# Kernel tuning notes

Hardware: AMD Instinct MI355X
Metric: run time of the kernel (lower is better)

Reference implementation:

```python
import jax, jax.numpy as jnp
import numpy as np

N, E = 50000, 800000          # n_nodes, n_edges
IN_C, OUT_C = 128, 64         # in_channels, out_channels


def setup_inputs() -> dict:
    key = jax.random.key(0)
    ks = jax.random.split(key, 12)
    def w(k, i, o):
        return jax.random.normal(k, (i, o), jnp.float32) / np.float32(np.sqrt(i))
    return {
        "x": jax.random.normal(ks[0], (N, IN_C), jnp.float32),
        "edge_index": jax.random.randint(ks[1], (2, E), 0, N),
        "eps": jax.random.normal(ks[2], (N, OUT_C), jnp.float32),
        # encoder GCNConv1: in -> 2*out
        "W_e1": w(ks[3], IN_C, 2 * OUT_C), "b_e1": jnp.zeros((2 * OUT_C,), jnp.float32),
        # encoder GCNConv2: 2*out -> out
        "W_e2": w(ks[4], 2 * OUT_C, OUT_C), "b_e2": jnp.zeros((OUT_C,), jnp.float32),
        # fc_mu / fc_logvar: out -> out
        "W_mu": w(ks[5], OUT_C, OUT_C), "b_mu": jnp.zeros((OUT_C,), jnp.float32),
        "W_lv": w(ks[6], OUT_C, OUT_C), "b_lv": jnp.zeros((OUT_C,), jnp.float32),
        # decoder GCNConv1: out -> in
        "W_d1": w(ks[7], OUT_C, IN_C), "b_d1": jnp.zeros((IN_C,), jnp.float32),
        # decoder GCNConv2: in -> in
        "W_d2": w(ks[8], IN_C, IN_C), "b_d2": jnp.zeros((IN_C,), jnp.float32),
    }


def _gcn_norm(edge_index, n):
    # PyG gcn_norm: add self-loops, symmetric D^-1/2 A D^-1/2 normalization
    loop = jnp.arange(n)
    src = jnp.concatenate([edge_index[0], loop])
    dst = jnp.concatenate([edge_index[1], loop])
    deg = jax.ops.segment_sum(jnp.ones_like(dst, jnp.float32), dst, num_segments=n)
    dinv = jnp.where(deg > 0, deg ** -0.5, 0.0)
    norm = dinv[src] * dinv[dst]  # [E + N]
    return src, dst, norm


def _gcn_conv(x, W, b, src, dst, norm, n):
    h = x @ W                       # linear transform first (small channel dim)
    msg = h[src] * norm[:, None]    # gather + edge scaling
    return jax.ops.segment_sum(msg, dst, num_segments=n) + b  # scatter-add + bias


def reference(x, edge_index, eps, W_e1, b_e1, W_e2, b_e2, W_mu, b_mu, W_lv, b_lv, W_d1, b_d1, W_d2, b_d2):
    n = x.shape[0]
    src, dst, norm = _gcn_norm(edge_index, n)
    # encoder
    h = jax.nn.relu(_gcn_conv(x, W_e1, b_e1, src, dst, norm, n))
    h = _gcn_conv(h, W_e2, b_e2, src, dst, norm, n)
    mu = h @ W_mu + b_mu
    logvar = h @ W_lv + b_lv
    # reparameterize (training mode)
    z = mu + eps * jnp.exp(0.5 * logvar)
    # decoder
    d = jax.nn.relu(_gcn_conv(z, W_d1, b_d1, src, dst, norm, n))
    d = _gcn_conv(d, W_d2, b_d2, src, dst, norm, n)
    return (d, mu, logvar)
```

## Files before the change

kernel.cpp:

```cpp
#include <hip/hip_runtime.h>
#include <math.h>

typedef unsigned short u16;
typedef unsigned int u32;
typedef __attribute__((ext_vector_type(8))) short s16x8;
typedef __attribute__((ext_vector_type(4))) float f32x4;

__device__ __forceinline__ float bf2f(u16 u) { return __uint_as_float(((u32)u) << 16); }
__device__ __forceinline__ u16 f2bf(float f) {
    u32 u = __float_as_uint(f);
    return (u16)((u + 0x7fffu + ((u >> 16) & 1u)) >> 16);
}

union U4 { u32 u[4]; s16x8 v; };

__device__ __forceinline__ s16x8 pack_hi(f32x4 x0, f32x4 x1) {
    U4 r;
    r.u[0] = (__float_as_uint(x0.y) & 0xFFFF0000u) | (__float_as_uint(x0.x) >> 16);
    r.u[1] = (__float_as_uint(x0.w) & 0xFFFF0000u) | (__float_as_uint(x0.z) >> 16);
    r.u[2] = (__float_as_uint(x1.y) & 0xFFFF0000u) | (__float_as_uint(x1.x) >> 16);
    r.u[3] = (__float_as_uint(x1.w) & 0xFFFF0000u) | (__float_as_uint(x1.z) >> 16);
    return r.v;
}
__device__ __forceinline__ s16x8 pack_lo(f32x4 x0, f32x4 x1) {
    float e0 = x0.x - __uint_as_float(__float_as_uint(x0.x) & 0xFFFF0000u);
    float e1 = x0.y - __uint_as_float(__float_as_uint(x0.y) & 0xFFFF0000u);
    float e2 = x0.z - __uint_as_float(__float_as_uint(x0.z) & 0xFFFF0000u);
    float e3 = x0.w - __uint_as_float(__float_as_uint(x0.w) & 0xFFFF0000u);
    float e4 = x1.x - __uint_as_float(__float_as_uint(x1.x) & 0xFFFF0000u);
    float e5 = x1.y - __uint_as_float(__float_as_uint(x1.y) & 0xFFFF0000u);
    float e6 = x1.z - __uint_as_float(__float_as_uint(x1.z) & 0xFFFF0000u);
    float e7 = x1.w - __uint_as_float(__float_as_uint(x1.w) & 0xFFFF0000u);
    U4 r;
    r.u[0] = (__float_as_uint(e1) & 0xFFFF0000u) | (__float_as_uint(e0) >> 16);
    r.u[1] = (__float_as_uint(e3) & 0xFFFF0000u) | (__float_as_uint(e2) >> 16);
    r.u[2] = (__float_as_uint(e5) & 0xFFFF0000u) | (__float_as_uint(e4) >> 16);
    r.u[3] = (__float_as_uint(e7) & 0xFFFF0000u) | (__float_as_uint(e6) >> 16);
    return r.v;
}

#define BSHIFT 9
#define BSIZE 512
#define BCAP 10240

struct PackArgs { const float* w[6]; };


__device__ __forceinline__ void pack_body(const PackArgs& pa, u16* __restrict__ out, int g, int t) {
    const int Ks[6] = {128, 128, 64, 64, 64, 128};
    const int Ms[6] = {128, 64, 64, 64, 128, 128};
    const int Off[6] = {0, 16384, 24576, 28672, 32768, 40960};
    int s = g >> 6;
    int id = (g & 63) * 256 + t;
    int K = Ks[s], M = Ms[s];
    if (id >= K * M) return;
    int ms = (M == 128) ? 7 : 6;
    int k = id >> ms, c = id & (M - 1);
    int chunk = k >> 5, j = k & 7, lq = (k >> 3) & 3;
    int ct = c >> 4, ln = (c & 15) + (lq << 4);
    out[Off[s] + (chunk * (M >> 4) + ct) * 512 + ln * 8 + j] = f2bf(pa.w[s][id]);
}


__global__ __launch_bounds__(256) void k_bin_pack(const int* __restrict__ ei, int E, int NB, int C,
                                                  int* __restrict__ bin_cursor, u32* __restrict__ binned,
                                                  PackArgs pa, u16* __restrict__ wpk) {
    __shared__ int sh[256];
    const int t = threadIdx.x;
    if ((int)blockIdx.x >= C) {
        pack_body(pa, wpk, blockIdx.x - C, t);
        return;
    }
    int* hist = sh;
    int* base_l = sh + 128;
    const int e0 = blockIdx.x * 4096;
    int sreg[16], dreg[16];
#pragma unroll
    for (int j = 0; j < 16; ++j) {
        int e = e0 + j * 256 + t;
        if (e < E) {
            sreg[j] = ei[e];
            dreg[j] = ei[E + e];
        } else {
            dreg[j] = -1;
        }
    }
    if (t < NB) hist[t] = 0;
    __syncthreads();
#pragma unroll
    for (int j = 0; j < 16; ++j)
        if (dreg[j] >= 0) atomicAdd(&hist[dreg[j] >> BSHIFT], 1);
    __syncthreads();
    if (t < NB) {
        base_l[t] = atomicAdd(&bin_cursor[t], hist[t]);
        hist[t] = 0;
    }
    __syncthreads();
#pragma unroll
    for (int j = 0; j < 16; ++j)
        if (dreg[j] >= 0) {
            int b = dreg[j] >> BSHIFT;
            int pos = base_l[b] + atomicAdd(&hist[b], 1);
            if (pos < BCAP) binned[(size_t)b * BCAP + pos] = ((u32)(dreg[j] & (BSIZE - 1)) << 17) | (u32)sreg[j];
        }
}


template <int K, int M, int RT, int NSET, bool XBF16, bool OUT_BF16, bool BREL>
__device__ __forceinline__ void gemm_tile(const void* __restrict__ Xv, const u16* __restrict__ Bpk,
                                          const float* __restrict__ b0, const float* __restrict__ b1,
                                          const float* __restrict__ eps,
                                          void* __restrict__ Y0, float* __restrict__ Y1,
                                          u16* __restrict__ Z, int N, int col0, int row0, int t) {
    constexpr int CH = K / 32;
    constexpr int TPM = M >> 4;
    constexpr int SETSTRIDE = CH * TPM * 512;
    const int lane = t & 63, w = t >> 6;
    const int l15 = lane & 15, q = lane >> 4;

    s16x8 Bfr[NSET * CH * 4];
#pragma unroll
    for (int s = 0; s < NSET; ++s)
#pragma unroll
        for (int ch = 0; ch < CH; ++ch)
#pragma unroll
            for (int ct = 0; ct < 4; ++ct)
                Bfr[(s * CH + ch) * 4 + ct] =
                    *(const s16x8*)&Bpk[(size_t)s * SETSTRIDE + ((ch * TPM) + (col0 >> 4) + ct) * 512 + lane * 8];

    f32x4 acc[NSET][RT][4];
#pragma unroll
    for (int s = 0; s < NSET; ++s)
#pragma unroll
        for (int rt = 0; rt < RT; ++rt)
#pragma unroll
            for (int ct = 0; ct < 4; ++ct) acc[s][rt][ct] = 0.f;

#pragma unroll
    for (int ch = 0; ch < CH; ++ch) {
#pragma unroll
        for (int rt = 0; rt < RT; ++rt) {
            int r = row0 + (w * RT + rt) * 16 + l15;
            r = r < N ? r : N - 1;
            s16x8 ah, al;
            if (XBF16) {
                ah = *(const s16x8*)((const u16*)Xv + (size_t)r * K + (ch << 5) + (q << 3));
            } else {
                const float* xp = (const float*)Xv + (size_t)r * K + (ch << 5) + (q << 3);
                f32x4 x0 = *(const f32x4*)xp;
                f32x4 x1 = *(const f32x4*)(xp + 4);
                ah = pack_hi(x0, x1);
                al = pack_lo(x0, x1);
            }
#pragma unroll
            for (int s = 0; s < NSET; ++s)
#pragma unroll
                for (int ct = 0; ct < 4; ++ct) {
                    int fb = (s * CH + ch) * 4 + ct;
                    acc[s][rt][ct] = __builtin_amdgcn_mfma_f32_16x16x32_bf16(ah, Bfr[fb], acc[s][rt][ct], 0, 0, 0);
                    if (!XBF16)
                        acc[s][rt][ct] = __builtin_amdgcn_mfma_f32_16x16x32_bf16(al, Bfr[fb], acc[s][rt][ct], 0, 0, 0);
                }
        }
    }

#pragma unroll
    for (int rt = 0; rt < RT; ++rt)
#pragma unroll
        for (int ct = 0; ct < 4; ++ct)
#pragma unroll
            for (int reg = 0; reg < 4; ++reg) {
                int row = row0 + (w * RT + rt) * 16 + q * 4 + reg;
                if (row >= N) continue;
                int col = col0 + ct * 16 + l15;
                if (NSET == 1) {
                    float v = acc[0][rt][ct][reg];
                    if (BREL) v = fmaxf(v + b0[col], 0.f);
                    if (OUT_BF16)
                        ((u16*)Y0)[(size_t)row * M + col] = f2bf(v);
                    else
                        ((float*)Y0)[(size_t)row * M + col] = v;
                } else {
                    float mu = acc[0][rt][ct][reg] + b0[col];
                    float lv = acc[1][rt][ct][reg] + b1[col];
                    size_t o = (size_t)row * 64 + col;
                    ((float*)Y0)[o] = mu;
                    Y1[o] = lv;
                    Z[o] = f2bf(mu + eps[o] * expf(0.5f * lv));
                }
            }
}

template <int K, int M, int RT, int NSET, bool XBF16, bool OUT_BF16, bool BREL>
__global__ __launch_bounds__(256, 3) void k_gemm(const void* __restrict__ Xv, const u16* __restrict__ Bpk,
                                                 const float* __restrict__ b0, const float* __restrict__ b1,
                                                 const float* __restrict__ eps,
                                                 void* __restrict__ Y0, float* __restrict__ Y1,
                                                 u16* __restrict__ Z, int N) {
    gemm_tile<K, M, RT, NSET, XBF16, OUT_BF16, BREL>(Xv, Bpk, b0, b1, eps, Y0, Y1, Z, N,
                                                     blockIdx.x * 64, blockIdx.y * (RT * 64), threadIdx.x);
}


__global__ __launch_bounds__(256, 3) void k_cnt_gemm1(const u32* __restrict__ binned,
                                                      const int* __restrict__ bin_cursor, int N, int NB,
                                                      int* __restrict__ cnt, float* __restrict__ dinv,
                                                      int* __restrict__ row_start, int* __restrict__ cursor,
                                                      const float* __restrict__ x, const u16* __restrict__ wpk,
                                                      u16* __restrict__ R1) {
    __shared__ int cnt_l[BSIZE];
    __shared__ int wave_sum[5];
    __shared__ int base_s;
    const int t = threadIdx.x;
    const int b = blockIdx.x;
    if (b >= NB) {
        gemm_tile<128, 128, 2, 1, false, true, false>(x, wpk, nullptr, nullptr, nullptr, R1, nullptr, nullptr,
                                                      N, 0, (b - NB) * 128, t);
        return;
    }
    const int lane = t & 63, w = t >> 6;
    cnt_l[t] = 0;
    cnt_l[t + 256] = 0;
    __syncthreads();
    const int n = min(bin_cursor[b], BCAP);
    for (int i = t; i < n; i += 256) atomicAdd(&cnt_l[binned[(size_t)b * BCAP + i] >> 17], 1);
    __syncthreads();
    int c0 = cnt_l[2 * t], c1 = cnt_l[2 * t + 1];
    int p0 = (c0 + 7) & ~7, p1 = (c1 + 7) & ~7;
    int s = p0 + p1;
    int incl = s;
#pragma unroll
    for (int o = 1; o < 64; o <<= 1) {
        int v = __shfl_up(incl, o, 64);
        if (lane >= o) incl += v;
    }
    if (lane == 63) wave_sum[w] = incl;
    __syncthreads();
    if (t == 0) {
        int acc = 0;
#pragma unroll
        for (int i = 0; i < 4; ++i) {
            int v = wave_sum[i];
            wave_sum[i] = acc;
            acc += v;
        }
        base_s = atomicAdd(cursor, acc);
    }
    __syncthreads();
    int excl = incl - s + wave_sum[w] + base_s;
    int v0 = b * BSIZE + 2 * t;
    if (v0 < N) {
        cnt[v0] = c0;
        dinv[v0] = rsqrtf((float)(c0 + 1));
        row_start[v0] = excl;
    }
    if (v0 + 1 < N) {
        cnt[v0 + 1] = c1;
        dinv[v0 + 1] = rsqrtf((float)(c1 + 1));
        row_start[v0 + 1] = excl + p0;
    }
}


__global__ __launch_bounds__(256, 3) void k_scat_gemm1(const u32* __restrict__ binned,
                                                       const int* __restrict__ bin_cursor,
                                                       const int* __restrict__ row_start,
                                                       const float* __restrict__ dinv, int N, int NB,
                                                       int2* __restrict__ edges,
                                                       const float* __restrict__ x, const u16* __restrict__ wpk,
                                                       u16* __restrict__ R1) {
    __shared__ float dv_l[BSIZE];
    __shared__ int rs_l[BSIZE];
    __shared__ int fill_l[BSIZE];
    const int t = threadIdx.x;
    const int b = blockIdx.x;
    if (b >= NB) {
        gemm_tile<128, 128, 2, 1, false, true, false>(x, wpk, nullptr, nullptr, nullptr, R1, nullptr, nullptr,
                                                      N, 64, (b - NB) * 128, t);
        return;
    }
#pragma unroll
    for (int hh = 0; hh < 2; ++hh) {
        int d = t + hh * 256;
        int v = b * BSIZE + d;
        bool ok = v < N;
        dv_l[d] = ok ? dinv[v] : 0.f;
        rs_l[d] = ok ? row_start[v] : 0;
        fill_l[d] = 0;
    }
    __syncthreads();
    const int n = min(bin_cursor[b], BCAP);
    for (int i = t; i < n; i += 256) {
        u32 e = binned[(size_t)b * BCAP + i];
        int dl = e >> 17;
        int src = e & 0x1FFFF;
        float wgt = dinv[src] * dv_l[dl];
        int pos = rs_l[dl] + atomicAdd(&fill_l[dl], 1);
        edges[pos] = make_int2(src, __float_as_int(wgt));
    }
    __syncthreads();
#pragma unroll
    for (int hh = 0; hh < 2; ++hh) {
        int d = t + hh * 256;
        int v = b * BSIZE + d;
        if (v >= N) continue;
        int c = fill_l[d];
        int pc = (c + 7) & ~7;
        for (int j = c; j < pc; ++j) edges[rs_l[d] + j] = make_int2(0, 0);
    }
}


template <bool RELU, bool OUT_BF16>
__global__ __launch_bounds__(256) void k_agg128(const u16* __restrict__ hin, const int2* __restrict__ edges,
                                                const int* __restrict__ row_start, const int* __restrict__ cnt,
                                                const float* __restrict__ dinv, const float* __restrict__ bias,
                                                void* __restrict__ out, int N) {
    const int v = blockIdx.x * 4 + (threadIdx.x >> 6);
    const int lane = threadIdx.x & 63;
    if (v >= N) return;
    const int start = __builtin_amdgcn_readfirstlane(row_start[v]);
    const int c = __builtin_amdgcn_readfirstlane(cnt[v]);
    const int pc = (c + 7) & ~7;
    const u32* hp = (const u32*)hin;
    float a0 = 0.f, a1 = 0.f;
    if (pc) {
        int2 e[8];
#pragma unroll
        for (int j = 0; j < 8; ++j) e[j] = edges[start + j];
        for (int i = 0; i < pc; i += 8) {
            u32 h[8];
            float wv[8];
#pragma unroll
            for (int j = 0; j < 8; ++j) {
                h[j] = hp[(size_t)e[j].x * 64 + lane];
                wv[j] = __int_as_float(e[j].y);
            }
            if (i + 8 < pc) {
#pragma unroll
                for (int j = 0; j < 8; ++j) e[j] = edges[start + i + 8 + j];
            }
#pragma unroll
            for (int j = 0; j < 8; ++j) {
                a0 = fmaf(wv[j], bf2f((u16)h[j]), a0);
                a1 = fmaf(wv[j], bf2f((u16)(h[j] >> 16)), a1);
            }
        }
    }
    float dv = dinv[v], sw = dv * dv;
    u32 hs = hp[(size_t)v * 64 + lane];
    a0 = fmaf(sw, bf2f((u16)hs), a0);
    a1 = fmaf(sw, bf2f((u16)(hs >> 16)), a1);
    float2 bp = ((const float2*)bias)[lane];
    a0 += bp.x;
    a1 += bp.y;
    if (RELU) { a0 = fmaxf(a0, 0.f); a1 = fmaxf(a1, 0.f); }
    if (OUT_BF16)
        ((u32*)out)[(size_t)v * 64 + lane] = (u32)f2bf(a0) | ((u32)f2bf(a1) << 16);
    else
        ((float2*)out)[(size_t)v * 64 + lane] = make_float2(a0, a1);
}

template <bool HASB>
__global__ __launch_bounds__(256) void k_agg64(const u16* __restrict__ hin, const int2* __restrict__ edges,
                                               const int* __restrict__ row_start, const int* __restrict__ cnt,
                                               const float* __restrict__ dinv, const float* __restrict__ bias,
                                               float* __restrict__ out, int N) {
    const int v = blockIdx.x * 4 + (threadIdx.x >> 6);
    const int lane = threadIdx.x & 63;
    if (v >= N) return;
    const int start = __builtin_amdgcn_readfirstlane(row_start[v]);
    const int c = __builtin_amdgcn_readfirstlane(cnt[v]);
    const int pc = (c + 7) & ~7;
    float a0 = 0.f;
    if (pc) {
        int2 e[8];
#pragma unroll
        for (int j = 0; j < 8; ++j) e[j] = edges[start + j];
        for (int i = 0; i < pc; i += 8) {
            u16 h[8];
            float wv[8];
#pragma unroll
            for (int j = 0; j < 8; ++j) {
                h[j] = hin[(size_t)e[j].x * 64 + lane];
                wv[j] = __int_as_float(e[j].y);
            }
            if (i + 8 < pc) {
#pragma unroll
                for (int j = 0; j < 8; ++j) e[j] = edges[start + i + 8 + j];
            }
#pragma unroll
            for (int j = 0; j < 8; ++j) a0 = fmaf(wv[j], bf2f(h[j]), a0);
        }
    }
    float dv = dinv[v];
    a0 = fmaf(dv * dv, bf2f(hin[(size_t)v * 64 + lane]), a0);
    if (HASB) a0 += bias[lane];
    out[(size_t)v * 64 + lane] = a0;
}


extern "C" void kernel_launch(void* const* d_in, const int* in_sizes, int n_in,
                              void* d_out, int out_size, void* d_ws, size_t ws_size,
                              hipStream_t stream) {
    const float* x = (const float*)d_in[0];
    const int* ei = (const int*)d_in[1];
    const float* eps = (const float*)d_in[2];
    const float* We1 = (const float*)d_in[3];
    const float* be1 = (const float*)d_in[4];
    const float* We2 = (const float*)d_in[5];
    const float* be2 = (const float*)d_in[6];
    const float* Wmu = (const float*)d_in[7];
    const float* bmu = (const float*)d_in[8];
    const float* Wlv = (const float*)d_in[9];
    const float* blv = (const float*)d_in[10];
    const float* Wd1 = (const float*)d_in[11];
    const float* bd1 = (const float*)d_in[12];
    const float* Wd2 = (const float*)d_in[13];
    const float* bd2 = (const float*)d_in[14];

    const int N = in_sizes[0] / 128;
    const int E = in_sizes[1] / 2;
    const int ECAP = E + 8 * N;
    const int NB = (N + BSIZE - 1) >> BSHIFT;
    const int C = (E + 4095) / 4096;

    int* bin_cursor = (int*)d_ws;
    int* cursor = bin_cursor + 128;
    float* dinv = (float*)(bin_cursor + 256);
    int* row_start = (int*)(dinv + N);
    int* cnt = row_start + N;
    int2* edges = (int2*)(cnt + N);
    u16* R1 = (u16*)(edges + ECAP);
    u16* AZu = R1 + (size_t)N * 128;
    u16* B2 = AZu + (size_t)N * 128;
    u16* Wpk = B2 + (size_t)N * 128;
    float* AZf = (float*)AZu;
    u32* binned = (u32*)AZu;

    float* out_d = (float*)d_out;
    float* out_mu = out_d + (size_t)N * 128;
    float* out_lv = out_mu + (size_t)N * 64;
    float* H2 = out_d;

    hipMemsetAsync(d_ws, 0, 256 * 4, stream);

    PackArgs pa;
    pa.w[0] = We1; pa.w[1] = We2; pa.w[2] = Wmu; pa.w[3] = Wlv; pa.w[4] = Wd1; pa.w[5] = Wd2;

    const int RB128 = (N + 127) / 128;
    const int RB64 = (N + 63) / 64;
    const int AB = (N + 3) / 4;

    k_bin_pack<<<dim3(C + 384), dim3(256), 0, stream>>>(ei, E, NB, C, bin_cursor, binned, pa, Wpk);
    k_cnt_gemm1<<<dim3(NB + RB128), dim3(256), 0, stream>>>(binned, bin_cursor, N, NB, cnt, dinv, row_start,
                                                            cursor, x, Wpk, R1);
    k_scat_gemm1<<<dim3(NB + RB128), dim3(256), 0, stream>>>(binned, bin_cursor, row_start, dinv, N, NB,
                                                             edges, x, Wpk, R1);
    k_agg128<true, true><<<dim3(AB), dim3(256), 0, stream>>>(R1, edges, row_start, cnt, dinv, be1, AZu, N);
    k_gemm<128, 64, 1, 1, true, true, false><<<dim3(1, RB64), dim3(256), 0, stream>>>(AZu, Wpk + 16384, nullptr, nullptr, nullptr, R1, nullptr, nullptr, N);
    k_agg64<true><<<dim3(AB), dim3(256), 0, stream>>>(R1, edges, row_start, cnt, dinv, be2, H2, N);
    k_gemm<64, 64, 1, 2, false, false, false><<<dim3(1, RB64), dim3(256), 0, stream>>>(H2, Wpk + 24576, bmu, blv, eps, out_mu, out_lv, R1, N);
    k_agg64<false><<<dim3(AB), dim3(256), 0, stream>>>(R1, edges, row_start, cnt, dinv, nullptr, AZf, N);
    k_gemm<64, 128, 2, 1, false, true, true><<<dim3(2, RB128), dim3(256), 0, stream>>>(AZf, Wpk + 32768, bd1, nullptr, nullptr, B2, nullptr, nullptr, N);
    k_gemm<128, 128, 2, 1, true, true, false><<<dim3(2, RB128), dim3(256), 0, stream>>>(B2, Wpk + 40960, nullptr, nullptr, nullptr, R1, nullptr, nullptr, N);
    k_agg128<false, false><<<dim3(AB), dim3(256), 0, stream>>>(R1, edges, row_start, cnt, dinv, bd2, out_d, N);
}
```

Baseline: 327.7 us.

## Replace per-node wave aggregation with channel-sliced multi-node aggregation kernel

Merges the two GCN aggregation kernels into one templated kernel. Each wavefront now handles four nodes at once, 16 lanes per node, and the feature channels are split across blocks in 64-byte slices. The intent is to put more independent row gathers in flight per wave and to let the 64-channel layers use packed 32-bit loads instead of 16-bit loads. It drops the software prefetch of edge records and the scalar (readfirstlane) edge indexing, so edge loads become per-lane and nodes in one wave can diverge on degree.

```diff
diff --git a/kernel.cpp b/kernel.cpp
--- a/kernel.cpp
+++ b/kernel.cpp
@@ -311,92 +311,58 @@
 }
 
 
-template <bool RELU, bool OUT_BF16>
-__global__ __launch_bounds__(256) void k_agg128(const u16* __restrict__ hin, const int2* __restrict__ edges,
-                                                const int* __restrict__ row_start, const int* __restrict__ cnt,
-                                                const float* __restrict__ dinv, const float* __restrict__ bias,
-                                                void* __restrict__ out, int N) {
-    const int v = blockIdx.x * 4 + (threadIdx.x >> 6);
-    const int lane = threadIdx.x & 63;
-    if (v >= N) return;
-    const int start = __builtin_amdgcn_readfirstlane(row_start[v]);
-    const int c = __builtin_amdgcn_readfirstlane(cnt[v]);
-    const int pc = (c + 7) & ~7;
+template <int CHU, int SL, bool RELU, bool OUT_BF16, bool HASB>
+__global__ __launch_bounds__(256) void k_aggs(const u16* __restrict__ hin, const int2* __restrict__ edges,
+                                              const int* __restrict__ row_start, const int* __restrict__ cnt,
+                                              const float* __restrict__ dinv, const float* __restrict__ bias,
+                                              void* __restrict__ out, int N) {
+    const int t = threadIdx.x;
+    const int w = t >> 6, l = t & 63;
+    const int sub = l >> 4, li = l & 15;
+    const int slice = (int)blockIdx.x % SL;
+    const int g = (int)blockIdx.x / SL;
+    const int v = g * 16 + w * 4 + sub;
+    const int off = slice * 16 + li;
     const u32* hp = (const u32*)hin;
+    const bool ok = v < N;
+    int start = 0, pc = 0;
+    if (ok) {
+        start = row_start[v];
+        pc = (cnt[v] + 7) & ~7;
+    }
     float a0 = 0.f, a1 = 0.f;
-    if (pc) {
+    for (int i = 0; i < pc; i += 8) {
         int2 e[8];
 #pragma unroll
-        for (int j = 0; j < 8; ++j) e[j] = edges[start + j];
-        for (int i = 0; i < pc; i += 8) {
-            u32 h[8];
-            float wv[8];
-#pragma unroll
-            for (int j = 0; j < 8; ++j) {
-                h[j] = hp[(size_t)e[j].x * 64 + lane];
-                wv[j] = __int_as_float(e[j].y);
-            }
-            if (i + 8 < pc) {
-#pragma unroll
-                for (int j = 0; j < 8; ++j) e[j] = edges[start + i + 8 + j];
-            }
-#pragma unroll
-            for (int j = 0; j < 8; ++j) {
-                a0 = fmaf(wv[j], bf2f((u16)h[j]), a0);
-                a1 = fmaf(wv[j], bf2f((u16)(h[j] >> 16)), a1);
-            }
+        for (int j = 0; j < 8; ++j) e[j] = edges[start + i + j];
+        u32 h[8];
+#pragma unroll
+        for (int j = 0; j < 8; ++j) h[j] = hp[(u32)e[j].x * CHU + off];
+#pragma unroll
+        for (int j = 0; j < 8; ++j) {
+            float wv = __int_as_float(e[j].y);
+            a0 = fmaf(wv, __uint_as_float(h[j] << 16), a0);
+            a1 = fmaf(wv, __uint_as_float(h[j] & 0xFFFF0000u), a1);
         }
     }
+    if (!ok) return;
     float dv = dinv[v], sw = dv * dv;
-    u32 hs = hp[(size_t)v * 64 + lane];
-    a0 = fmaf(sw, bf2f((u16)hs), a0);
-    a1 = fmaf(sw, bf2f((u16)(hs >> 16)), a1);
-    float2 bp = ((const float2*)bias)[lane];
-    a0 += bp.x;
-    a1 += bp.y;
-    if (RELU) { a0 = fmaxf(a0, 0.f); a1 = fmaxf(a1, 0.f); }
+    u32 hs = hp[(u32)v * CHU + off];
+    a0 = fmaf(sw, __uint_as_float(hs << 16), a0);
+    a1 = fmaf(sw, __uint_as_float(hs & 0xFFFF0000u), a1);
+    if (HASB) {
+        float2 bp = ((const float2*)bias)[off];
+        a0 += bp.x;
+        a1 += bp.y;
+    }
+    if (RELU) {
+        a0 = fmaxf(a0, 0.f);
+        a1 = fmaxf(a1, 0.f);
+    }
     if (OUT_BF16)
-        ((u32*)out)[(size_t)v * 64 + lane] = (u32)f2bf(a0) | ((u32)f2bf(a1) << 16);
+        ((u32*)out)[(size_t)v * CHU + off] = (u32)f2bf(a0) | ((u32)f2bf(a1) << 16);
     else
-        ((float2*)out)[(size_t)v * 64 + lane] = make_float2(a0, a1);
-}
-
-template <bool HASB>
-__global__ __launch_bounds__(256) void k_agg64(const u16* __restrict__ hin, const int2* __restrict__ edges,
-                                               const int* __restrict__ row_start, const int* __restrict__ cnt,
-                                               const float* __restrict__ dinv, const float* __restrict__ bias,
-                                               float* __restrict__ out, int N) {
-    const int v = blockIdx.x * 4 + (threadIdx.x >> 6);
-    const int lane = threadIdx.x & 63;
-    if (v >= N) return;
-    const int start = __builtin_amdgcn_readfirstlane(row_start[v]);
-    const int c = __builtin_amdgcn_readfirstlane(cnt[v]);
-    const int pc = (c + 7) & ~7;
-    float a0 = 0.f;
-    if (pc) {
-        int2 e[8];
-#pragma unroll
-        for (int j = 0; j < 8; ++j) e[j] = edges[start + j];
-        for (int i = 0; i < pc; i += 8) {
-            u16 h[8];
-            float wv[8];
-#pragma unroll
-            for (int j = 0; j < 8; ++j) {
-                h[j] = hin[(size_t)e[j].x * 64 + lane];
-                wv[j] = __int_as_float(e[j].y);
-            }
-            if (i + 8 < pc) {
-#pragma unroll
-                for (int j = 0; j < 8; ++j) e[j] = edges[start + i + 8 + j];
-            }
-#pragma unroll
-            for (int j = 0; j < 8; ++j) a0 = fmaf(wv[j], bf2f(h[j]), a0);
-        }
-    }
-    float dv = dinv[v];
-    a0 = fmaf(dv * dv, bf2f(hin[(size_t)v * 64 + lane]), a0);
-    if (HASB) a0 += bias[lane];
-    out[(size_t)v * 64 + lane] = a0;
+        ((float2*)out)[(size_t)v * CHU + off] = make_float2(a0, a1);
 }
 
 
@@ -450,19 +416,19 @@
 
     const int RB128 = (N + 127) / 128;
     const int RB64 = (N + 63) / 64;
-    const int AB = (N + 3) / 4;
+    const int GB = (N + 15) / 16;
 
     k_bin_pack<<<dim3(C + 384), dim3(256), 0, stream>>>(ei, E, NB, C, bin_cursor, binned, pa, Wpk);
     k_cnt_gemm1<<<dim3(NB + RB128), dim3(256), 0, stream>>>(binned, bin_cursor, N, NB, cnt, dinv, row_start,
                                                             cursor, x, Wpk, R1);
     k_scat_gemm1<<<dim3(NB + RB128), dim3(256), 0, stream>>>(binned, bin_cursor, row_start, dinv, N, NB,
                                                              edges, x, Wpk, R1);
-    k_agg128<true, true><<<dim3(AB), dim3(256), 0, stream>>>(R1, edges, row_start, cnt, dinv, be1, AZu, N);
+    k_aggs<64, 4, true, true, true><<<dim3(4 * GB), dim3(256), 0, stream>>>(R1, edges, row_start, cnt, dinv, be1, AZu, N);
     k_gemm<128, 64, 1, 1, true, true, false><<<dim3(1, RB64), dim3(256), 0, stream>>>(AZu, Wpk + 16384, nullptr, nullptr, nullptr, R1, nullptr, nullptr, N);
-    k_agg64<true><<<dim3(AB), dim3(256), 0, stream>>>(R1, edges, row_start, cnt, dinv, be2, H2, N);
+    k_aggs<32, 2, false, false, true><<<dim3(2 * GB), dim3(256), 0, stream>>>(R1, edges, row_start, cnt, dinv, be2, H2, N);
     k_gemm<64, 64, 1, 2, false, false, false><<<dim3(1, RB64), dim3(256), 0, stream>>>(H2, Wpk + 24576, bmu, blv, eps, out_mu, out_lv, R1, N);
-    k_agg64<false><<<dim3(AB), dim3(256), 0, stream>>>(R1, edges, row_start, cnt, dinv, nullptr, AZf, N);
+    k_aggs<32, 2, false, false, false><<<dim3(2 * GB), dim3(256), 0, stream>>>(R1, edges, row_start, cnt, dinv, nullptr, AZf, N);
     k_gemm<64, 128, 2, 1, false, true, true><<<dim3(2, RB128), dim3(256), 0, stream>>>(AZf, Wpk + 32768, bd1, nullptr, nullptr, B2, nullptr, nullptr, N);
     k_gemm<128, 128, 2, 1, true, true, false><<<dim3(2, RB128), dim3(256), 0, stream>>>(B2, Wpk + 40960, nullptr, nullptr, nullptr, R1, nullptr, nullptr, N);
-    k_agg128<false, false><<<dim3(AB), dim3(256), 0, stream>>>(R1, edges, row_start, cnt, dinv, bd2, out_d, N);
-}
+    k_aggs<64, 4, false, false, true><<<dim3(4 * GB), dim3(256), 0, stream>>>(R1, edges, row_start, cnt, dinv, bd2, out_d, N);
+}
```

Result: slower. 342.5 us (+4.5%).

## Fuse each aggregation with the following dense GEMMs into per-16-row kernels

Applied to the files above, without the earlier changes.

Each neighbour aggregation now writes its 16-row tile into shared memory and immediately runs the next linear layer(s) with MFMA in the same block. This covers conv2's W, the mu/logvar heads plus reparameterisation, and both decoder GEMMs. The standalone k_gemm launches and the global round trips of the intermediate activations go away, cutting the launch count from 10 to 7. In exchange, the gather phase uses 16-row blocks that need a barrier, and the GEMM tiles are tiny (one MFMA tile per wave), so per-block efficiency may drop.

```diff
diff --git a/kernel.cpp b/kernel.cpp
--- a/kernel.cpp
+++ b/kernel.cpp
@@ -173,32 +173,13 @@
                 int row = row0 + (w * RT + rt) * 16 + q * 4 + reg;
                 if (row >= N) continue;
                 int col = col0 + ct * 16 + l15;
-                if (NSET == 1) {
-                    float v = acc[0][rt][ct][reg];
-                    if (BREL) v = fmaxf(v + b0[col], 0.f);
-                    if (OUT_BF16)
-                        ((u16*)Y0)[(size_t)row * M + col] = f2bf(v);
-                    else
-                        ((float*)Y0)[(size_t)row * M + col] = v;
-                } else {
-                    float mu = acc[0][rt][ct][reg] + b0[col];
-                    float lv = acc[1][rt][ct][reg] + b1[col];
-                    size_t o = (size_t)row * 64 + col;
-                    ((float*)Y0)[o] = mu;
-                    Y1[o] = lv;
-                    Z[o] = f2bf(mu + eps[o] * expf(0.5f * lv));
-                }
+                float v = acc[0][rt][ct][reg];
+                if (BREL) v = fmaxf(v + b0[col], 0.f);
+                if (OUT_BF16)
+                    ((u16*)Y0)[(size_t)row * M + col] = f2bf(v);
+                else
+                    ((float*)Y0)[(size_t)row * M + col] = v;
             }
-}
-
-template <int K, int M, int RT, int NSET, bool XBF16, bool OUT_BF16, bool BREL>
-__global__ __launch_bounds__(256, 3) void k_gemm(const void* __restrict__ Xv, const u16* __restrict__ Bpk,
-                                                 const float* __restrict__ b0, const float* __restrict__ b1,
-                                                 const float* __restrict__ eps,
-                                                 void* __restrict__ Y0, float* __restrict__ Y1,
-                                                 u16* __restrict__ Z, int N) {
-    gemm_tile<K, M, RT, NSET, XBF16, OUT_BF16, BREL>(Xv, Bpk, b0, b1, eps, Y0, Y1, Z, N,
-                                                     blockIdx.x * 64, blockIdx.y * (RT * 64), threadIdx.x);
 }
 
 
@@ -311,11 +292,243 @@
 }
 
 
-template <bool RELU, bool OUT_BF16>
-__global__ __launch_bounds__(256) void k_agg128(const u16* __restrict__ hin, const int2* __restrict__ edges,
-                                                const int* __restrict__ row_start, const int* __restrict__ cnt,
-                                                const float* __restrict__ dinv, const float* __restrict__ bias,
-                                                void* __restrict__ out, int N) {
+__device__ __forceinline__ void agg_row128(const u32* __restrict__ hp, const int2* __restrict__ edges,
+                                           int start, int pc, int lane, float& a0, float& a1) {
+    if (!pc) return;
+    int2 e[8];
+#pragma unroll
+    for (int j = 0; j < 8; ++j) e[j] = edges[start + j];
+    for (int i = 0; i < pc; i += 8) {
+        u32 h[8];
+        float wv[8];
+#pragma unroll
+        for (int j = 0; j < 8; ++j) {
+            h[j] = hp[(size_t)e[j].x * 64 + lane];
+            wv[j] = __int_as_float(e[j].y);
+        }
+        if (i + 8 < pc) {
+#pragma unroll
+            for (int j = 0; j < 8; ++j) e[j] = edges[start + i + 8 + j];
+        }
+#pragma unroll
+        for (int j = 0; j < 8; ++j) {
+            a0 = fmaf(wv[j], bf2f((u16)h[j]), a0);
+            a1 = fmaf(wv[j], bf2f((u16)(h[j] >> 16)), a1);
+        }
+    }
+}
+
+__device__ __forceinline__ void agg_row64(const u16* __restrict__ hin, const int2* __restrict__ edges,
+                                          int start, int pc, int lane, float& a0) {
+    if (!pc) return;
+    int2 e[8];
+#pragma unroll
+    for (int j = 0; j < 8; ++j) e[j] = edges[start + j];
+    for (int i = 0; i < pc; i += 8) {
+        u16 h[8];
+        float wv[8];
+#pragma unroll
+        for (int j = 0; j < 8; ++j) {
+            h[j] = hin[(size_t)e[j].x * 64 + lane];
+            wv[j] = __int_as_float(e[j].y);
+        }
+        if (i + 8 < pc) {
+#pragma unroll
+            for (int j = 0; j < 8; ++j) e[j] = edges[start + i + 8 + j];
+        }
+#pragma unroll
+        for (int j = 0; j < 8; ++j) a0 = fmaf(wv[j], bf2f(h[j]), a0);
+    }
+}
+
+
+__global__ __launch_bounds__(256) void k_agg1_g2(const u16* __restrict__ R1, const int2* __restrict__ edges,
+                                                 const int* __restrict__ row_start, const int* __restrict__ cnt,
+                                                 const float* __restrict__ dinv, const float* __restrict__ be1,
+                                                 const u16* __restrict__ Bpk, u16* __restrict__ W1, int N) {
+    __shared__ u16 Ar[16 * 136];
+    const int t = threadIdx.x, w = t >> 6, lane = t & 63;
+    const u32* hp = (const u32*)R1;
+#pragma unroll
+    for (int i = 0; i < 4; ++i) {
+        const int r = w * 4 + i;
+        const int v = blockIdx.x * 16 + r;
+        float a0 = 0.f, a1 = 0.f;
+        if (v < N) {
+            const int start = __builtin_amdgcn_readfirstlane(row_start[v]);
+            const int c = __builtin_amdgcn_readfirstlane(cnt[v]);
+            const int pc = (c + 7) & ~7;
+            agg_row128(hp, edges, start, pc, lane, a0, a1);
+            float dv = dinv[v], sw = dv * dv;
+            u32 hs = hp[(size_t)v * 64 + lane];
+            a0 = fmaf(sw, bf2f((u16)hs), a0);
+            a1 = fmaf(sw, bf2f((u16)(hs >> 16)), a1);
+            float2 bp = ((const float2*)be1)[lane];
+            a0 += bp.x;
+            a1 += bp.y;
+            a0 = fmaxf(a0, 0.f);
+            a1 = fmaxf(a1, 0.f);
+        }
+        ((u32*)Ar)[r * 68 + lane] = (u32)f2bf(a0) | ((u32)f2bf(a1) << 16);
+    }
+    __syncthreads();
+    const int l15 = lane & 15, q = lane >> 4;
+    f32x4 acc = 0.f;
+#pragma unroll
+    for (int ch = 0; ch < 4; ++ch) {
+        s16x8 ah = *(const s16x8*)&Ar[l15 * 136 + ch * 32 + q * 8];
+        s16x8 b = *(const s16x8*)&Bpk[(ch * 4 + w) * 512 + lane * 8];
+        acc = __builtin_amdgcn_mfma_f32_16x16x32_bf16(ah, b, acc, 0, 0, 0);
+    }
+#pragma unroll
+    for (int reg = 0; reg < 4; ++reg) {
+        int row = blockIdx.x * 16 + q * 4 + reg;
+        if (row >= N) continue;
+        int col = w * 16 + l15;
+        W1[(size_t)row * 64 + col] = f2bf(acc[reg]);
+    }
+}
+
+
+__global__ __launch_bounds__(256) void k_agg2_mlv(const u16* __restrict__ W1, const int2* __restrict__ edges,
+                                                  const int* __restrict__ row_start, const int* __restrict__ cnt,
+                                                  const float* __restrict__ dinv, const float* __restrict__ be2,
+                                                  const u16* __restrict__ Bmu, const u16* __restrict__ Blv,
+                                                  const float* __restrict__ bmu, const float* __restrict__ blv,
+                                                  const float* __restrict__ eps,
+                                                  float* __restrict__ out_mu, float* __restrict__ out_lv,
+                                                  u16* __restrict__ Zb, int N) {
+    __shared__ float Af[16 * 68];
+    const int t = threadIdx.x, w = t >> 6, lane = t & 63;
+#pragma unroll
+    for (int i = 0; i < 4; ++i) {
+        const int r = w * 4 + i;
+        const int v = blockIdx.x * 16 + r;
+        float a0 = 0.f;
+        if (v < N) {
+            const int start = __builtin_amdgcn_readfirstlane(row_start[v]);
+            const int c = __builtin_amdgcn_readfirstlane(cnt[v]);
+            const int pc = (c + 7) & ~7;
+            agg_row64(W1, edges, start, pc, lane, a0);
+            float dv = dinv[v];
+            a0 = fmaf(dv * dv, bf2f(W1[(size_t)v * 64 + lane]), a0);
+            a0 += be2[lane];
+        }
+        Af[r * 68 + lane] = a0;
+    }
+    __syncthreads();
+    const int l15 = lane & 15, q = lane >> 4;
+    f32x4 accm = 0.f, accl = 0.f;
+#pragma unroll
+    for (int ch = 0; ch < 2; ++ch) {
+        f32x4 x0 = *(const f32x4*)&Af[l15 * 68 + ch * 32 + q * 8];
+        f32x4 x1 = *(const f32x4*)&Af[l15 * 68 + ch * 32 + q * 8 + 4];
+        s16x8 ah = pack_hi(x0, x1);
+        s16x8 al = pack_lo(x0, x1);
+        s16x8 bm = *(const s16x8*)&Bmu[(ch * 4 + w) * 512 + lane * 8];
+        s16x8 bl = *(const s16x8*)&Blv[(ch * 4 + w) * 512 + lane * 8];
+        accm = __builtin_amdgcn_mfma_f32_16x16x32_bf16(ah, bm, accm, 0, 0, 0);
+        accm = __builtin_amdgcn_mfma_f32_16x16x32_bf16(al, bm, accm, 0, 0, 0);
+        accl = __builtin_amdgcn_mfma_f32_16x16x32_bf16(ah, bl, accl, 0, 0, 0);
+        accl = __builtin_amdgcn_mfma_f32_16x16x32_bf16(al, bl, accl, 0, 0, 0);
+    }
+#pragma unroll
+    for (int reg = 0; reg < 4; ++reg) {
+        int row = blockIdx.x * 16 + q * 4 + reg;
+        if (row >= N) continue;
+        int col = w * 16 + l15;
+        size_t o = (size_t)row * 64 + col;
+        float mu = accm[reg] + bmu[col];
+        float lv = accl[reg] + blv[col];
+        out_mu[o] = mu;
+        out_lv[o] = lv;
+        Zb[o] = f2bf(mu + eps[o] * expf(0.5f * lv));
+    }
+}
+
+
+__global__ __launch_bounds__(256) void k_agg3_d12(const u16* __restrict__ Zb, const int2* __restrict__ edges,
+                                                  const int* __restrict__ row_start, const int* __restrict__ cnt,
+                                                  const float* __restrict__ dinv,
+                                                  const u16* __restrict__ Bd1, const u16* __restrict__ Bd2,
+                                                  const float* __restrict__ bd1, u16* __restrict__ R1, int N) {
+    __shared__ float Zr[16 * 68];
+    __shared__ u16 Br[16 * 136];
+    const int t = threadIdx.x, w = t >> 6, lane = t & 63;
+#pragma unroll
+    for (int i = 0; i < 4; ++i) {
+        const int r = w * 4 + i;
+        const int v = blockIdx.x * 16 + r;
+        float a0 = 0.f;
+        if (v < N) {
+            const int start = __builtin_amdgcn_readfirstlane(row_start[v]);
+            const int c = __builtin_amdgcn_readfirstlane(cnt[v]);
+            const int pc = (c + 7) & ~7;
+            agg_row64(Zb, edges, start, pc, lane, a0);
+            float dv = dinv[v];
+            a0 = fmaf(dv * dv, bf2f(Zb[(size_t)v * 64 + lane]), a0);
+        }
+        Zr[r * 68 + lane] = a0;
+    }
+    __syncthreads();
+    const int l15 = lane & 15, q = lane >> 4;
+    {
+        f32x4 acc1[2];
+        acc1[0] = 0.f;
+        acc1[1] = 0.f;
+#pragma unroll
+        for (int ch = 0; ch < 2; ++ch) {
+            f32x4 x0 = *(const f32x4*)&Zr[l15 * 68 + ch * 32 + q * 8];
+            f32x4 x1 = *(const f32x4*)&Zr[l15 * 68 + ch * 32 + q * 8 + 4];
+            s16x8 ah = pack_hi(x0, x1);
+            s16x8 al = pack_lo(x0, x1);
+#pragma unroll
+            for (int cti = 0; cti < 2; ++cti) {
+                s16x8 b = *(const s16x8*)&Bd1[(ch * 8 + w + cti * 4) * 512 + lane * 8];
+                acc1[cti] = __builtin_amdgcn_mfma_f32_16x16x32_bf16(ah, b, acc1[cti], 0, 0, 0);
+                acc1[cti] = __builtin_amdgcn_mfma_f32_16x16x32_bf16(al, b, acc1[cti], 0, 0, 0);
+            }
+        }
+#pragma unroll
+        for (int cti = 0; cti < 2; ++cti)
+#pragma unroll
+            for (int reg = 0; reg < 4; ++reg) {
+                int col = (w + cti * 4) * 16 + l15;
+                float v = fmaxf(acc1[cti][reg] + bd1[col], 0.f);
+                Br[(q * 4 + reg) * 136 + col] = f2bf(v);
+            }
+    }
+    __syncthreads();
+    {
+        f32x4 acc2[2];
+        acc2[0] = 0.f;
+        acc2[1] = 0.f;
+#pragma unroll
+        for (int ch = 0; ch < 4; ++ch) {
+            s16x8 ah = *(const s16x8*)&Br[l15 * 136 + ch * 32 + q * 8];
+#pragma unroll
+            for (int cti = 0; cti < 2; ++cti) {
+                s16x8 b = *(const s16x8*)&Bd2[(ch * 8 + w + cti * 4) * 512 + lane * 8];
+                acc2[cti] = __builtin_amdgcn_mfma_f32_16x16x32_bf16(ah, b, acc2[cti], 0, 0, 0);
+            }
+        }
+#pragma unroll
+        for (int cti = 0; cti < 2; ++cti)
+#pragma unroll
+            for (int reg = 0; reg < 4; ++reg) {
+                int row = blockIdx.x * 16 + q * 4 + reg;
+                if (row >= N) continue;
+                int col = (w + cti * 4) * 16 + l15;
+                R1[(size_t)row * 128 + col] = f2bf(acc2[cti][reg]);
+            }
+    }
+}
+
+
+__global__ __launch_bounds__(256) void k_agg4(const u16* __restrict__ hin, const int2* __restrict__ edges,
+                                              const int* __restrict__ row_start, const int* __restrict__ cnt,
+                                              const float* __restrict__ dinv, const float* __restrict__ bias,
+                                              float* __restrict__ out, int N) {
     const int v = blockIdx.x * 4 + (threadIdx.x >> 6);
     const int lane = threadIdx.x & 63;
     if (v >= N) return;
@@ -324,29 +537,7 @@
     const int pc = (c + 7) & ~7;
     const u32* hp = (const u32*)hin;
     float a0 = 0.f, a1 = 0.f;
-    if (pc) {
-        int2 e[8];
-#pragma unroll
-        for (int j = 0; j < 8; ++j) e[j] = edges[start + j];
-        for (int i = 0; i < pc; i += 8) {
-            u32 h[8];
-            float wv[8];
-#pragma unroll
-            for (int j = 0; j < 8; ++j) {
-                h[j] = hp[(size_t)e[j].x * 64 + lane];
-                wv[j] = __int_as_float(e[j].y);
-            }
-            if (i + 8 < pc) {
-#pragma unroll
-                for (int j = 0; j < 8; ++j) e[j] = edges[start + i + 8 + j];
-            }
-#pragma unroll
-            for (int j = 0; j < 8; ++j) {
-                a0 = fmaf(wv[j], bf2f((u16)h[j]), a0);
-                a1 = fmaf(wv[j], bf2f((u16)(h[j] >> 16)), a1);
-            }
-        }
-    }
+    agg_row128(hp, edges, start, pc, lane, a0, a1);
     float dv = dinv[v], sw = dv * dv;
     u32 hs = hp[(size_t)v * 64 + lane];
     a0 = fmaf(sw, bf2f((u16)hs), a0);
@@ -354,49 +545,7 @@
     float2 bp = ((const float2*)bias)[lane];
     a0 += bp.x;
     a1 += bp.y;
-    if (RELU) { a0 = fmaxf(a0, 0.f); a1 = fmaxf(a1, 0.f); }
-    if (OUT_BF16)
-        ((u32*)out)[(size_t)v * 64 + lane] = (u32)f2bf(a0) | ((u32)f2bf(a1) << 16);
-    else
-        ((float2*)out)[(size_t)v * 64 + lane] = make_float2(a0, a1);
-}
-
-template <bool HASB>
-__global__ __launch_bounds__(256) void k_agg64(const u16* __restrict__ hin, const int2* __restrict__ edges,
-                                               const int* __restrict__ row_start, const int* __restrict__ cnt,
-                                               const float* __restrict__ dinv, const float* __restrict__ bias,
-                                               float* __restrict__ out, int N) {
-    const int v = blockIdx.x * 4 + (threadIdx.x >> 6);
-    const int lane = threadIdx.x & 63;
-    if (v >= N) return;
-    const int start = __builtin_amdgcn_readfirstlane(row_start[v]);
-    const int c = __builtin_amdgcn_readfirstlane(cnt[v]);
-    const int pc = (c + 7) & ~7;
-    float a0 = 0.f;
-    if (pc) {
-        int2 e[8];
-#pragma unroll
-        for (int j = 0; j < 8; ++j) e[j] = edges[start + j];
-        for (int i = 0; i < pc; i += 8) {
-            u16 h[8];
-            float wv[8];
-#pragma unroll
-            for (int j = 0; j < 8; ++j) {
-                h[j] = hin[(size_t)e[j].x * 64 + lane];
-                wv[j] = __int_as_float(e[j].y);
-            }
-            if (i + 8 < pc) {
-#pragma unroll
-                for (int j = 0; j < 8; ++j) e[j] = edges[start + i + 8 + j];
-            }
-#pragma unroll
-            for (int j = 0; j < 8; ++j) a0 = fmaf(wv[j], bf2f(h[j]), a0);
-        }
-    }
-    float dv = dinv[v];
-    a0 = fmaf(dv * dv, bf2f(hin[(size_t)v * 64 + lane]), a0);
-    if (HASB) a0 += bias[lane];
-    out[(size_t)v * 64 + lane] = a0;
+    ((float2*)out)[(size_t)v * 64 + lane] = make_float2(a0, a1);
 }
 
 
@@ -432,16 +581,14 @@
     int* cnt = row_start + N;
     int2* edges = (int2*)(cnt + N);
     u16* R1 = (u16*)(edges + ECAP);
-    u16* AZu = R1 + (size_t)N * 128;
-    u16* B2 = AZu + (size_t)N * 128;
-    u16* Wpk = B2 + (size_t)N * 128;
-    float* AZf = (float*)AZu;
-    u32* binned = (u32*)AZu;
+    u16* W1 = R1 + (size_t)N * 128;
+    u16* Zb = W1 + (size_t)N * 128;
+    u16* Wpk = Zb + (size_t)N * 128;
+    u32* binned = (u32*)W1;
 
     float* out_d = (float*)d_out;
     float* out_mu = out_d + (size_t)N * 128;
     float* out_lv = out_mu + (size_t)N * 64;
-    float* H2 = out_d;
 
     hipMemsetAsync(d_ws, 0, 256 * 4, stream);
 
@@ -449,20 +596,18 @@
     pa.w[0] = We1; pa.w[1] = We2; pa.w[2] = Wmu; pa.w[3] = Wlv; pa.w[4] = Wd1; pa.w[5] = Wd2;
 
     const int RB128 = (N + 127) / 128;
-    const int RB64 = (N + 63) / 64;
     const int AB = (N + 3) / 4;
+    const int FB = (N + 15) / 16;
 
     k_bin_pack<<<dim3(C + 384), dim3(256), 0, stream>>>(ei, E, NB, C, bin_cursor, binned, pa, Wpk);
     k_cnt_gemm1<<<dim3(NB + RB128), dim3(256), 0, stream>>>(binned, bin_cursor, N, NB, cnt, dinv, row_start,
                                                             cursor, x, Wpk, R1);
     k_scat_gemm1<<<dim3(NB + RB128), dim3(256), 0, stream>>>(binned, bin_cursor, row_start, dinv, N, NB,
                                                              edges, x, Wpk, R1);
-    k_agg128<true, true><<<dim3(AB), dim3(256), 0, stream>>>(R1, edges, row_start, cnt, dinv, be1, AZu, N);
-    k_gemm<128, 64, 1, 1, true, true, false><<<dim3(1, RB64), dim3(256), 0, stream>>>(AZu, Wpk + 16384, nullptr, nullptr, nullptr, R1, nullptr, nullptr, N);
-    k_agg64<true><<<dim3(AB), dim3(256), 0, stream>>>(R1, edges, row_start, cnt, dinv, be2, H2, N);
-    k_gemm<64, 64, 1, 2, false, false, false><<<dim3(1, RB64), dim3(256), 0, stream>>>(H2, Wpk + 24576, bmu, blv, eps, out_mu, out_lv, R1, N);
-    k_agg64<false><<<dim3(AB), dim3(256), 0, stream>>>(R1, edges, row_start, cnt, dinv, nullptr, AZf, N);
-    k_gemm<64, 128, 2, 1, false, true, true><<<dim3(2, RB128), dim3(256), 0, stream>>>(AZf, Wpk + 32768, bd1, nullptr, nullptr, B2, nullptr, nullptr, N);
-    k_gemm<128, 128, 2, 1, true, true, false><<<dim3(2, RB128), dim3(256), 0, stream>>>(B2, Wpk + 40960, nullptr, nullptr, nullptr, R1, nullptr, nullptr, N);
-    k_agg128<false, false><<<dim3(AB), dim3(256), 0, stream>>>(R1, edges, row_start, cnt, dinv, bd2, out_d, N);
-}
+    k_agg1_g2<<<dim3(FB), dim3(256), 0, stream>>>(R1, edges, row_start, cnt, dinv, be1, Wpk + 16384, W1, N);
+    k_agg2_mlv<<<dim3(FB), dim3(256), 0, stream>>>(W1, edges, row_start, cnt, dinv, be2, Wpk + 24576,
+                                                   Wpk + 28672, bmu, blv, eps, out_mu, out_lv, Zb, N);
+    k_agg3_d12<<<dim3(FB), dim3(256), 0, stream>>>(Zb, edges, row_start, cnt, dinv, Wpk + 32768,
+                                                   Wpk + 40960, bd1, R1, N);
+    k_agg4<<<dim3(AB), dim3(256), 0, stream>>>(R1, edges, row_start, cnt, dinv, bd2, out_d, N);
+}
```

Result: faster. 299.8 us (-8.5%).
